# Performance work log

Hardware: AMD Instinct MI355X
Metric: run time of the kernel (lower is better)

The kernel has to match this reference:

```python
import jax, jax.numpy as jnp
import numpy as np

N, E = 50000, 800000
DIN, DH, DOUT = 128, 128, 64


def setup_inputs() -> dict:
    key = jax.random.key(0)
    k = jax.random.split(key, 6)
    node_features = jax.random.normal(k[0], (N, DIN), dtype=jnp.float32)
    edge_src = jax.random.randint(k[1], (E,), 0, N)
    edge_dst = jax.random.randint(k[2], (E,), 0, N)
    # Glorot-ish init for the two GCNConv weight matrices, zero bias (PyG default bias=True)
    W1 = jax.random.normal(k[3], (DIN, DH), dtype=jnp.float32) * (1.0 / np.sqrt(DIN))
    b1 = jnp.zeros((DH,), dtype=jnp.float32)
    W2 = jax.random.normal(k[4], (DH, DOUT), dtype=jnp.float32) * (1.0 / np.sqrt(DH))
    b2 = jnp.zeros((DOUT,), dtype=jnp.float32)
    return {"node_features": node_features, "edge_src": edge_src, "edge_dst": edge_dst,
            "W1": W1, "b1": b1, "W2": W2, "b2": b2}


def gcn_conv(x, W, b, src, dst, n):
    """PyG GCNConv: add self-loops, symmetric D^-1/2 (A+I) D^-1/2 normalization."""
    xw = x @ W  # [n, d_out]
    loops = jnp.arange(n, dtype=src.dtype)
    s = jnp.concatenate([src, loops])  # edges + self-loops
    d = jnp.concatenate([dst, loops])
    deg = jax.ops.segment_sum(jnp.ones_like(d, dtype=xw.dtype), d, num_segments=n)
    dinv = jnp.where(deg > 0, jax.lax.rsqrt(deg), 0.0)
    norm = dinv[s] * dinv[d]  # [E + n]
    msg = xw[s] * norm[:, None]  # gather + scale (memory-bound)
    out = jax.ops.segment_sum(msg, d, num_segments=n)  # scatter-add
    return out + b


def reference(node_features, edge_src, edge_dst, W1, b1, W2, b2):
    n = node_features.shape[0]
    h = gcn_conv(node_features, W1, b1, edge_src, edge_dst, n)
    h = jax.nn.relu(h)  # dropout omitted (inference / eval mode)
    h = gcn_conv(h, W2, b2, edge_src, edge_dst, n)
    # EdgePredictor: per-edge dot product of endpoint representations
    score = jnp.sum(h[edge_src] * h[edge_dst], axis=-1)  # [E]
    return score
```

## Files before the change

kernel.cpp:

```cpp
#include <hip/hip_runtime.h>
#include <hip/hip_bf16.h>
#include <type_traits>


#define DIN 128
#define DH  128
#define DOUT 64
#define BSH 7
#define BNODES 128
#define CAP 2560
#define QSH 13
#define POISON 0xAAAAAAAAu

typedef __attribute__((ext_vector_type(8))) short short8;
typedef __attribute__((ext_vector_type(4))) float floatx4;

__device__ inline float2 bf2_to_f2(unsigned u) {
    union { unsigned i; float f; } a, b;
    a.i = u << 16;
    b.i = u & 0xffff0000u;
    return make_float2(a.f, b.f);
}
__device__ inline float bf_to_f(unsigned short u) {
    union { unsigned i; float f; } a;
    a.i = ((unsigned)u) << 16;
    return a.f;
}
__device__ inline unsigned short f_to_bf(float f) {
    union { float f; unsigned i; } v; v.f = f;
    unsigned r = v.i + 0x7fffu + ((v.i >> 16) & 1u);
    return (unsigned short)(r >> 16);
}

__global__ __launch_bounds__(256) void place_gemm1_kernel(
    const int* __restrict__ src, const int* __restrict__ dst,
    unsigned* __restrict__ cursor, uint2* __restrict__ tmp, int E, int EB,
    const float* __restrict__ X, const float* __restrict__ W1,
    unsigned short* __restrict__ Y, int nrows) {
    __shared__ __align__(16) char smem[69632];
    int bid = blockIdx.x, t = threadIdx.x;

    if (bid < EB) {
        int* hist = (int*)smem;
        int* cur  = hist + 512;
        hist[t] = 0; hist[t + 256] = 0;
        __syncthreads();
        int base = bid * 4096 + t;
        int d[16];
#pragma unroll
        for (int it = 0; it < 16; ++it) {
            int e = base + it * 256;
            d[it] = (e < E) ? dst[e] : -1;
            if (d[it] >= 0) atomicAdd(&hist[d[it] >> BSH], 1);
        }
        __syncthreads();
#pragma unroll
        for (int k = t; k < 512; k += 256)
            if (hist[k])
                cur[k] = (int)(atomicAdd(&cursor[k], (unsigned)hist[k]) - POISON);
        __syncthreads();
#pragma unroll
        for (int it = 0; it < 16; ++it) {
            int e = base + it * 256;
            if (d[it] >= 0) {
                int bkt = d[it] >> BSH;
                int r = atomicAdd(&cur[bkt], 1);
                if (r >= 0 && r < CAP)
                    tmp[(size_t)bkt * CAP + r] =
                        make_uint2((unsigned)src[e] |
                                   ((unsigned)(d[it] & (BNODES - 1)) << 16),
                                   (unsigned)e);
            }
        }
        return;
    }

    constexpr int KP = 136;
    unsigned short* Xs = (unsigned short*)smem;
    unsigned short* Wt = Xs + 128 * KP;
    int row0 = (bid - EB) * 128;

#pragma unroll
    for (int it = 0; it < 16; ++it) {
        int idx = it * 256 + t;
        int r = idx >> 5;
        int c4 = (idx & 31) * 4;
        int gr = row0 + r; if (gr >= nrows) gr = nrows - 1;
        float4 v = *(const float4*)(X + (size_t)gr * 128 + c4);
        ushort4 p;
        p.x = f_to_bf(v.x); p.y = f_to_bf(v.y);
        p.z = f_to_bf(v.z); p.w = f_to_bf(v.w);
        *(ushort4*)&Xs[r * KP + c4] = p;
    }
#pragma unroll
    for (int it = 0; it < 16; ++it) {
        int idx = it * 256 + t;
        int n = idx >> 5;
        int k4 = (idx & 31) * 4;
        ushort4 p;
        p.x = f_to_bf(W1[(size_t)(k4 + 0) * 128 + n]);
        p.y = f_to_bf(W1[(size_t)(k4 + 1) * 128 + n]);
        p.z = f_to_bf(W1[(size_t)(k4 + 2) * 128 + n]);
        p.w = f_to_bf(W1[(size_t)(k4 + 3) * 128 + n]);
        *(ushort4*)&Wt[n * KP + k4] = p;
    }
    __syncthreads();

    int wv = t >> 6, lane = t & 63;
    int lr = lane & 15;
    int lk = (lane >> 4) * 8;
    int rw = wv * 32;

    floatx4 acc[2][8];
#pragma unroll
    for (int rt = 0; rt < 2; ++rt)
#pragma unroll
        for (int ct = 0; ct < 8; ++ct) acc[rt][ct] = (floatx4){0.f, 0.f, 0.f, 0.f};

#pragma unroll
    for (int kk = 0; kk < 128; kk += 32) {
        short8 a[2], b[8];
#pragma unroll
        for (int rt = 0; rt < 2; ++rt)
            a[rt] = *(const short8*)&Xs[(rw + rt * 16 + lr) * KP + kk + lk];
#pragma unroll
        for (int ct = 0; ct < 8; ++ct)
            b[ct] = *(const short8*)&Wt[(ct * 16 + lr) * KP + kk + lk];
#pragma unroll
        for (int rt = 0; rt < 2; ++rt)
#pragma unroll
            for (int ct = 0; ct < 8; ++ct)
                acc[rt][ct] = __builtin_amdgcn_mfma_f32_16x16x32_bf16(
                    a[rt], b[ct], acc[rt][ct], 0, 0, 0);
    }
#pragma unroll
    for (int rt = 0; rt < 2; ++rt) {
#pragma unroll
        for (int i = 0; i < 4; ++i) {
            int grow = row0 + rw + rt * 16 + (lane >> 4) * 4 + i;
            if (grow >= nrows) continue;
#pragma unroll
            for (int ct = 0; ct < 8; ++ct)
                Y[(size_t)grow * 128 + ct * 16 + lr] = f_to_bf(acc[rt][ct][i]);
        }
    }
}

__global__ __launch_bounds__(256) void bucket_csr_kernel(const uint2* __restrict__ tmp,
                                                         const unsigned* __restrict__ cursor,
                                                         int* __restrict__ row_beg,
                                                         int* __restrict__ row_end,
                                                         float* __restrict__ dinv,
                                                         int* __restrict__ col,
                                                         int* __restrict__ eidx, int N) {
    __shared__ int hist[1024], cur[1024];
    __shared__ int tsum[256];
    __shared__ unsigned ebuf[CAP];
    __shared__ unsigned ibuf[CAP];
    __shared__ unsigned ssrc[CAP];
    __shared__ unsigned sidx[CAP];
    int b = blockIdx.x, t = threadIdx.x;
    int size = (int)(cursor[b] - POISON);
    if (size < 0) size = 0;
    if (size > CAP) size = CAP;
    size_t rbase = (size_t)b * CAP;
#pragma unroll
    for (int k = 0; k < 4; ++k) hist[t * 4 + k] = 0;
    __syncthreads();
    for (int i = t; i < size; i += 256) {
        uint2 e = tmp[rbase + i];
        ebuf[i] = e.x;
        ibuf[i] = e.y;
        int key = (int)(e.x >> 16) * 8 + (int)((e.x & 0xffffu) >> QSH);
        atomicAdd(&hist[key], 1);
    }
    __syncthreads();
    int local[4];
    int s = 0;
#pragma unroll
    for (int k = 0; k < 4; ++k) { local[k] = hist[t * 4 + k]; s += local[k]; }
    tsum[t] = s;
    __syncthreads();
    for (int off = 1; off < 256; off <<= 1) {
        int u = (t >= off) ? tsum[t - off] : 0;
        __syncthreads();
        tsum[t] += u;
        __syncthreads();
    }
    int run = tsum[t] - s;
#pragma unroll
    for (int k = 0; k < 4; ++k) {
        hist[t * 4 + k] = run;
        cur[t * 4 + k] = run;
        run += local[k];
    }
    __syncthreads();
    if (t < BNODES) {
        int node = b * BNODES + t;
        if (node < N) {
            int nbeg = hist[t * 8];
            int nend = (t == BNODES - 1) ? size : hist[t * 8 + 8];
            row_beg[node] = (int)rbase + nbeg;
            row_end[node] = (int)rbase + nend;
            dinv[node] = rsqrtf((float)(nend - nbeg + 1));
        }
    }
    __syncthreads();
    for (int i = t; i < size; i += 256) {
        unsigned e = ebuf[i];
        int key = (int)(e >> 16) * 8 + (int)((e & 0xffffu) >> QSH);
        int r = atomicAdd(&cur[key], 1);
        ssrc[r] = e & 0xffffu;
        sidx[r] = ibuf[i];
    }
    __syncthreads();
    for (int i = t; i < size; i += 256) {
        col[rbase + i]  = (int)ssrc[i];
        eidx[rbase + i] = (int)sidx[i];
    }
}

__global__ __launch_bounds__(256) void agg1_kernel(const unsigned short* __restrict__ y1,
                                                   const int* __restrict__ row_beg,
                                                   const int* __restrict__ row_end,
                                                   const int* __restrict__ col,
                                                   const float* __restrict__ dinv,
                                                   const float* __restrict__ b1,
                                                   unsigned short* __restrict__ h1, int n) {
    int w = (blockIdx.x * 256 + threadIdx.x) >> 6;
    int lane = threadIdx.x & 63;
    if (w >= n) return;
    float dw = dinv[w];
    float acc0, acc1;
    {
        float2 t2 = bf2_to_f2(*(const unsigned*)(y1 + (size_t)w * 128 + lane * 2));
        acc0 = dw * t2.x; acc1 = dw * t2.y;
    }
    int beg = row_beg[w], end = row_end[w];
    int i = beg;
    for (; i + 8 <= end; i += 8) {
        int s[8];
#pragma unroll
        for (int u = 0; u < 8; ++u) s[u] = col[i + u];
        float dv[8];
#pragma unroll
        for (int u = 0; u < 8; ++u) dv[u] = dinv[s[u]];
        unsigned tv[8];
#pragma unroll
        for (int u = 0; u < 8; ++u)
            tv[u] = *(const unsigned*)(y1 + (size_t)s[u] * 128 + lane * 2);
#pragma unroll
        for (int u = 0; u < 8; ++u) {
            float2 f = bf2_to_f2(tv[u]);
            acc0 = fmaf(dv[u], f.x, acc0);
            acc1 = fmaf(dv[u], f.y, acc1);
        }
    }
    for (; i < end; ++i) {
        int s = col[i];
        float dv = dinv[s];
        float2 f = bf2_to_f2(*(const unsigned*)(y1 + (size_t)s * 128 + lane * 2));
        acc0 = fmaf(dv, f.x, acc0);
        acc1 = fmaf(dv, f.y, acc1);
    }
    float r0 = fmaxf(fmaf(dw, acc0, b1[lane * 2]), 0.f);
    float r1 = fmaxf(fmaf(dw, acc1, b1[lane * 2 + 1]), 0.f);
    unsigned pk = (unsigned)f_to_bf(r0) | ((unsigned)f_to_bf(r1) << 16);
    *(unsigned*)(h1 + (size_t)w * 128 + lane * 2) = pk;
}

__global__ __launch_bounds__(256) void mfma_gemm2_kernel(const unsigned short* __restrict__ X,
                                                         const float* __restrict__ W,
                                                         const float* __restrict__ dinv,
                                                         unsigned short* __restrict__ Y,
                                                         int nrows) {
    constexpr int KP = 136;
    __shared__ unsigned short Xs[128 * KP];
    __shared__ unsigned short Wt[64 * KP];
    int tid = threadIdx.x;
    int row0 = blockIdx.x * 128;

#pragma unroll
    for (int it = 0; it < 8; ++it) {
        int idx = it * 256 + tid;
        int r = idx >> 4;
        int c8 = (idx & 15) * 8;
        int gr = row0 + r; if (gr >= nrows) gr = nrows - 1;
        uint4 v = *(const uint4*)(X + (size_t)gr * 128 + c8);
        *(uint4*)&Xs[r * KP + c8] = v;
    }
#pragma unroll
    for (int it = 0; it < 8; ++it) {
        int idx = it * 256 + tid;
        int n = idx >> 5;
        int k4 = (idx & 31) * 4;
        ushort4 p;
        p.x = f_to_bf(W[(size_t)(k4 + 0) * 64 + n]);
        p.y = f_to_bf(W[(size_t)(k4 + 1) * 64 + n]);
        p.z = f_to_bf(W[(size_t)(k4 + 2) * 64 + n]);
        p.w = f_to_bf(W[(size_t)(k4 + 3) * 64 + n]);
        *(ushort4*)&Wt[n * KP + k4] = p;
    }
    __syncthreads();

    int wv = tid >> 6, lane = tid & 63;
    int lr = lane & 15;
    int lk = (lane >> 4) * 8;
    int rw = wv * 32;

    floatx4 acc[2][4];
#pragma unroll
    for (int rt = 0; rt < 2; ++rt)
#pragma unroll
        for (int ct = 0; ct < 4; ++ct) acc[rt][ct] = (floatx4){0.f, 0.f, 0.f, 0.f};

#pragma unroll
    for (int kk = 0; kk < 128; kk += 32) {
        short8 a[2], b[4];
#pragma unroll
        for (int rt = 0; rt < 2; ++rt)
            a[rt] = *(const short8*)&Xs[(rw + rt * 16 + lr) * KP + kk + lk];
#pragma unroll
        for (int ct = 0; ct < 4; ++ct)
            b[ct] = *(const short8*)&Wt[(ct * 16 + lr) * KP + kk + lk];
#pragma unroll
        for (int rt = 0; rt < 2; ++rt)
#pragma unroll
            for (int ct = 0; ct < 4; ++ct)
                acc[rt][ct] = __builtin_amdgcn_mfma_f32_16x16x32_bf16(
                    a[rt], b[ct], acc[rt][ct], 0, 0, 0);
    }
#pragma unroll
    for (int rt = 0; rt < 2; ++rt) {
#pragma unroll
        for (int i = 0; i < 4; ++i) {
            int grow = row0 + rw + rt * 16 + (lane >> 4) * 4 + i;
            if (grow >= nrows) continue;
            float dv = dinv[grow];
#pragma unroll
            for (int ct = 0; ct < 4; ++ct)
                Y[(size_t)grow * 64 + ct * 16 + lr] = f_to_bf(acc[rt][ct][i] * dv);
        }
    }
}

__global__ __launch_bounds__(256) void agg2_kernel(const unsigned short* __restrict__ y,
                                                   const int* __restrict__ row_beg,
                                                   const int* __restrict__ row_end,
                                                   const int* __restrict__ col,
                                                   const float* __restrict__ dinv,
                                                   const float* __restrict__ bias,
                                                   unsigned short* __restrict__ out, int n) {
    int w = (blockIdx.x * 256 + threadIdx.x) >> 6;
    int lane = threadIdx.x & 63;
    if (w >= n) return;
    float acc = bf_to_f(y[(size_t)w * 64 + lane]);
    int beg = row_beg[w], end = row_end[w];
    int i = beg;
    for (; i + 8 <= end; i += 8) {
        int s[8];
#pragma unroll
        for (int u = 0; u < 8; ++u) s[u] = col[i + u];
        unsigned short tv[8];
#pragma unroll
        for (int u = 0; u < 8; ++u) tv[u] = y[(size_t)s[u] * 64 + lane];
#pragma unroll
        for (int u = 0; u < 8; ++u) acc += bf_to_f(tv[u]);
    }
    for (; i < end; ++i) acc += bf_to_f(y[(size_t)col[i] * 64 + lane]);
    float r = fmaf(dinv[w], acc, bias[lane]);
    out[(size_t)w * 64 + lane] = f_to_bf(r);
}

__global__ __launch_bounds__(256) void score_csr_kernel(const unsigned short* __restrict__ h2,
                                                        const int* __restrict__ row_beg,
                                                        const int* __restrict__ row_end,
                                                        const int* __restrict__ col,
                                                        const int* __restrict__ eidx,
                                                        float* __restrict__ out, int n) {
    int w = (blockIdx.x * 256 + threadIdx.x) >> 6;
    int lane = threadIdx.x & 63;
    if (w >= n) return;
    int q = lane & 7;
    uint4 hd = *(const uint4*)(h2 + (size_t)w * 64 + q * 8);
    float d0[8];
    { float2 f;
      f = bf2_to_f2(hd.x); d0[0] = f.x; d0[1] = f.y;
      f = bf2_to_f2(hd.y); d0[2] = f.x; d0[3] = f.y;
      f = bf2_to_f2(hd.z); d0[4] = f.x; d0[5] = f.y;
      f = bf2_to_f2(hd.w); d0[6] = f.x; d0[7] = f.y; }
    int beg = row_beg[w], end = row_end[w];
    int g = lane >> 3;
    for (int i = beg; i < end; i += 8) {
        int ei = i + g;
        bool ok = ei < end;
        int s = ok ? col[ei] : 0;
        uint4 hs = *(const uint4*)(h2 + (size_t)s * 64 + q * 8);
        float v = 0.f;
        float2 f;
        f = bf2_to_f2(hs.x); v = fmaf(d0[0], f.x, v); v = fmaf(d0[1], f.y, v);
        f = bf2_to_f2(hs.y); v = fmaf(d0[2], f.x, v); v = fmaf(d0[3], f.y, v);
        f = bf2_to_f2(hs.z); v = fmaf(d0[4], f.x, v); v = fmaf(d0[5], f.y, v);
        f = bf2_to_f2(hs.w); v = fmaf(d0[6], f.x, v); v = fmaf(d0[7], f.y, v);
        v += __shfl_xor(v, 4);
        v += __shfl_xor(v, 2);
        v += __shfl_xor(v, 1);
        if (ok && q == 0) out[eidx[ei]] = v;
    }
}

extern "C" void kernel_launch(void* const* d_in, const int* in_sizes, int n_in,
                              void* d_out, int out_size, void* d_ws, size_t ws_size,
                              hipStream_t stream) {
    const float* X   = (const float*)d_in[0];
    const int*   src = (const int*)d_in[1];
    const int*   dst = (const int*)d_in[2];
    const float* W1  = (const float*)d_in[3];
    const float* b1  = (const float*)d_in[4];
    const float* W2  = (const float*)d_in[5];
    const float* b2  = (const float*)d_in[6];
    float* score = (float*)d_out;

    const int N = in_sizes[0] / DIN;
    const int E = in_sizes[1];
    const int nbuck = (N + BNODES - 1) / BNODES;
    const int EB = (E + 4095) / 4096;
    const int GB = (N + 127) / 128;

    auto align = [](size_t x) { return (x + 255) & ~(size_t)255; };
    char* p = (char*)d_ws;
    unsigned* cursor = (unsigned*)p;        p += align(512 * 4);
    int*   row_beg = (int*)p;               p += align((size_t)N * 4);
    int*   row_end = (int*)p;               p += align((size_t)N * 4);
    float* dinv    = (float*)p;             p += align((size_t)N * 4);
    int*   col     = (int*)p;               p += align((size_t)nbuck * CAP * 4);
    int*   eidx    = (int*)p;               p += align((size_t)nbuck * CAP * 4);
    uint2* tmp     = (uint2*)p;             p += align((size_t)nbuck * CAP * 8);
    unsigned short* y1 = (unsigned short*)p; p += align((size_t)N * DH * 2);
    unsigned short* h1 = (unsigned short*)p; p += align((size_t)N * DH * 2);
    unsigned short* y2 = y1;
    unsigned short* h2 = y1 + (size_t)N * DOUT;

    place_gemm1_kernel<<<EB + GB, 256, 0, stream>>>(src, dst, cursor, tmp, E, EB,
                                                    X, W1, y1, N);
    bucket_csr_kernel<<<nbuck, 256, 0, stream>>>(tmp, cursor, row_beg, row_end,
                                                 dinv, col, eidx, N);

    int agg_blocks = (N + 3) / 4;
    agg1_kernel<<<agg_blocks, 256, 0, stream>>>(y1, row_beg, row_end, col,
                                                dinv, b1, h1, N);

    mfma_gemm2_kernel<<<GB, 256, 0, stream>>>(h1, W2, dinv, y2, N);

    agg2_kernel<<<agg_blocks, 256, 0, stream>>>(y2, row_beg, row_end, col,
                                                dinv, b2, h2, N);
    score_csr_kernel<<<agg_blocks, 256, 0, stream>>>(h2, row_beg, row_end,
                                                     col, eidx, score, N);
}
```

Baseline: 233.2 us.

## Fuse CSR bucket build with first-layer aggregation using global degree atomics

The per-bucket CSR construction kernel and the layer-1 aggregation kernel become one 512-thread kernel. Each block aggregates its own 128 destination nodes straight from the sorted source list still in LDS, instead of reading col back from global memory. Source-node normalisation needs degrees from other buckets, so the placement kernel now also keeps a global per-node in-degree counter with atomics, and source dinv is recomputed on the fly. This removes one launch and one round trip of CSR data through global memory. The cost is extra global atomics in the placement kernel and far fewer blocks for the aggregation work, each wave walking 16 nodes in sequence.

```diff
diff --git a/kernel.cpp b/kernel.cpp
--- a/kernel.cpp
+++ b/kernel.cpp
@@ -34,7 +34,8 @@
 
 __global__ __launch_bounds__(256) void place_gemm1_kernel(
     const int* __restrict__ src, const int* __restrict__ dst,
-    unsigned* __restrict__ cursor, uint2* __restrict__ tmp, int E, int EB,
+    unsigned* __restrict__ cursor, unsigned* __restrict__ deg,
+    uint2* __restrict__ tmp, int E, int EB,
     const float* __restrict__ X, const float* __restrict__ W1,
     unsigned short* __restrict__ Y, int nrows) {
     __shared__ __align__(16) char smem[69632];
@@ -51,7 +52,10 @@
         for (int it = 0; it < 16; ++it) {
             int e = base + it * 256;
             d[it] = (e < E) ? dst[e] : -1;
-            if (d[it] >= 0) atomicAdd(&hist[d[it] >> BSH], 1);
+            if (d[it] >= 0) {
+                atomicAdd(&hist[d[it] >> BSH], 1);
+                atomicAdd(&deg[d[it]], 1u);
+            }
         }
         __syncthreads();
 #pragma unroll
@@ -146,15 +150,15 @@
     }
 }
 
-__global__ __launch_bounds__(256) void bucket_csr_kernel(const uint2* __restrict__ tmp,
-                                                         const unsigned* __restrict__ cursor,
-                                                         int* __restrict__ row_beg,
-                                                         int* __restrict__ row_end,
-                                                         float* __restrict__ dinv,
-                                                         int* __restrict__ col,
-                                                         int* __restrict__ eidx, int N) {
+__global__ __launch_bounds__(512) void csr_agg1_kernel(
+    const uint2* __restrict__ tmp, const unsigned* __restrict__ cursor,
+    const unsigned* __restrict__ deg,
+    int* __restrict__ row_beg, int* __restrict__ row_end,
+    float* __restrict__ dinv, int* __restrict__ col, int* __restrict__ eidx,
+    const unsigned short* __restrict__ y1, const float* __restrict__ b1,
+    unsigned short* __restrict__ h1, int N) {
     __shared__ int hist[1024], cur[1024];
-    __shared__ int tsum[256];
+    __shared__ int tsum[512];
     __shared__ unsigned ebuf[CAP];
     __shared__ unsigned ibuf[CAP];
     __shared__ unsigned ssrc[CAP];
@@ -164,10 +168,9 @@
     if (size < 0) size = 0;
     if (size > CAP) size = CAP;
     size_t rbase = (size_t)b * CAP;
-#pragma unroll
-    for (int k = 0; k < 4; ++k) hist[t * 4 + k] = 0;
-    __syncthreads();
-    for (int i = t; i < size; i += 256) {
+    hist[t] = 0; hist[t + 512] = 0;
+    __syncthreads();
+    for (int i = t; i < size; i += 512) {
         uint2 e = tmp[rbase + i];
         ebuf[i] = e.x;
         ibuf[i] = e.y;
@@ -175,25 +178,19 @@
         atomicAdd(&hist[key], 1);
     }
     __syncthreads();
-    int local[4];
-    int s = 0;
-#pragma unroll
-    for (int k = 0; k < 4; ++k) { local[k] = hist[t * 4 + k]; s += local[k]; }
+    int l0 = hist[t * 2], l1 = hist[t * 2 + 1];
+    int s = l0 + l1;
     tsum[t] = s;
     __syncthreads();
-    for (int off = 1; off < 256; off <<= 1) {
+    for (int off = 1; off < 512; off <<= 1) {
         int u = (t >= off) ? tsum[t - off] : 0;
         __syncthreads();
         tsum[t] += u;
         __syncthreads();
     }
     int run = tsum[t] - s;
-#pragma unroll
-    for (int k = 0; k < 4; ++k) {
-        hist[t * 4 + k] = run;
-        cur[t * 4 + k] = run;
-        run += local[k];
-    }
+    hist[t * 2] = run;       cur[t * 2] = run;
+    hist[t * 2 + 1] = run + l0; cur[t * 2 + 1] = run + l0;
     __syncthreads();
     if (t < BNODES) {
         int node = b * BNODES + t;
@@ -206,7 +203,7 @@
         }
     }
     __syncthreads();
-    for (int i = t; i < size; i += 256) {
+    for (int i = t; i < size; i += 512) {
         unsigned e = ebuf[i];
         int key = (int)(e >> 16) * 8 + (int)((e & 0xffffu) >> QSH);
         int r = atomicAdd(&cur[key], 1);
@@ -214,59 +211,55 @@
         sidx[r] = ibuf[i];
     }
     __syncthreads();
-    for (int i = t; i < size; i += 256) {
+    for (int i = t; i < size; i += 512) {
         col[rbase + i]  = (int)ssrc[i];
         eidx[rbase + i] = (int)sidx[i];
     }
-}
-
-__global__ __launch_bounds__(256) void agg1_kernel(const unsigned short* __restrict__ y1,
-                                                   const int* __restrict__ row_beg,
-                                                   const int* __restrict__ row_end,
-                                                   const int* __restrict__ col,
-                                                   const float* __restrict__ dinv,
-                                                   const float* __restrict__ b1,
-                                                   unsigned short* __restrict__ h1, int n) {
-    int w = (blockIdx.x * 256 + threadIdx.x) >> 6;
-    int lane = threadIdx.x & 63;
-    if (w >= n) return;
-    float dw = dinv[w];
-    float acc0, acc1;
-    {
-        float2 t2 = bf2_to_f2(*(const unsigned*)(y1 + (size_t)w * 128 + lane * 2));
-        acc0 = dw * t2.x; acc1 = dw * t2.y;
-    }
-    int beg = row_beg[w], end = row_end[w];
-    int i = beg;
-    for (; i + 8 <= end; i += 8) {
-        int s[8];
-#pragma unroll
-        for (int u = 0; u < 8; ++u) s[u] = col[i + u];
-        float dv[8];
-#pragma unroll
-        for (int u = 0; u < 8; ++u) dv[u] = dinv[s[u]];
-        unsigned tv[8];
-#pragma unroll
-        for (int u = 0; u < 8; ++u)
-            tv[u] = *(const unsigned*)(y1 + (size_t)s[u] * 128 + lane * 2);
-#pragma unroll
-        for (int u = 0; u < 8; ++u) {
-            float2 f = bf2_to_f2(tv[u]);
-            acc0 = fmaf(dv[u], f.x, acc0);
-            acc1 = fmaf(dv[u], f.y, acc1);
-        }
-    }
-    for (; i < end; ++i) {
-        int s = col[i];
-        float dv = dinv[s];
-        float2 f = bf2_to_f2(*(const unsigned*)(y1 + (size_t)s * 128 + lane * 2));
-        acc0 = fmaf(dv, f.x, acc0);
-        acc1 = fmaf(dv, f.y, acc1);
-    }
-    float r0 = fmaxf(fmaf(dw, acc0, b1[lane * 2]), 0.f);
-    float r1 = fmaxf(fmaf(dw, acc1, b1[lane * 2 + 1]), 0.f);
-    unsigned pk = (unsigned)f_to_bf(r0) | ((unsigned)f_to_bf(r1) << 16);
-    *(unsigned*)(h1 + (size_t)w * 128 + lane * 2) = pk;
+    int wv = t >> 6, lane = t & 63;
+    float bb0 = b1[lane * 2], bb1 = b1[lane * 2 + 1];
+    for (int l = wv; l < BNODES; l += 8) {
+        int node = b * BNODES + l;
+        if (node >= N) break;
+        int nbeg = hist[l * 8];
+        int nend = (l == BNODES - 1) ? size : hist[l * 8 + 8];
+        float dw = rsqrtf((float)(nend - nbeg + 1));
+        float acc0, acc1;
+        {
+            float2 t2 = bf2_to_f2(*(const unsigned*)(y1 + (size_t)node * 128 + lane * 2));
+            acc0 = dw * t2.x; acc1 = dw * t2.y;
+        }
+        int i = nbeg;
+        for (; i + 8 <= nend; i += 8) {
+            int s8[8];
+#pragma unroll
+            for (int u = 0; u < 8; ++u) s8[u] = (int)ssrc[i + u];
+            float dv[8];
+#pragma unroll
+            for (int u = 0; u < 8; ++u)
+                dv[u] = rsqrtf((float)((int)(deg[s8[u]] - POISON) + 1));
+            unsigned tv[8];
+#pragma unroll
+            for (int u = 0; u < 8; ++u)
+                tv[u] = *(const unsigned*)(y1 + (size_t)s8[u] * 128 + lane * 2);
+#pragma unroll
+            for (int u = 0; u < 8; ++u) {
+                float2 f = bf2_to_f2(tv[u]);
+                acc0 = fmaf(dv[u], f.x, acc0);
+                acc1 = fmaf(dv[u], f.y, acc1);
+            }
+        }
+        for (; i < nend; ++i) {
+            int sv = (int)ssrc[i];
+            float dv = rsqrtf((float)((int)(deg[sv] - POISON) + 1));
+            float2 f = bf2_to_f2(*(const unsigned*)(y1 + (size_t)sv * 128 + lane * 2));
+            acc0 = fmaf(dv, f.x, acc0);
+            acc1 = fmaf(dv, f.y, acc1);
+        }
+        float r0 = fmaxf(fmaf(dw, acc0, bb0), 0.f);
+        float r1 = fmaxf(fmaf(dw, acc1, bb1), 0.f);
+        unsigned pk = (unsigned)f_to_bf(r0) | ((unsigned)f_to_bf(r1) << 16);
+        *(unsigned*)(h1 + (size_t)node * 128 + lane * 2) = pk;
+    }
 }
 
 __global__ __launch_bounds__(256) void mfma_gemm2_kernel(const unsigned short* __restrict__ X,
@@ -430,6 +423,7 @@
     auto align = [](size_t x) { return (x + 255) & ~(size_t)255; };
     char* p = (char*)d_ws;
     unsigned* cursor = (unsigned*)p;        p += align(512 * 4);
+    unsigned* deg    = (unsigned*)p;        p += align((size_t)N * 4);
     int*   row_beg = (int*)p;               p += align((size_t)N * 4);
     int*   row_end = (int*)p;               p += align((size_t)N * 4);
     float* dinv    = (float*)p;             p += align((size_t)N * 4);
@@ -441,17 +435,14 @@
     unsigned short* y2 = y1;
     unsigned short* h2 = y1 + (size_t)N * DOUT;
 
-    place_gemm1_kernel<<<EB + GB, 256, 0, stream>>>(src, dst, cursor, tmp, E, EB,
-                                                    X, W1, y1, N);
-    bucket_csr_kernel<<<nbuck, 256, 0, stream>>>(tmp, cursor, row_beg, row_end,
-                                                 dinv, col, eidx, N);
+    place_gemm1_kernel<<<EB + GB, 256, 0, stream>>>(src, dst, cursor, deg, tmp,
+                                                    E, EB, X, W1, y1, N);
+    csr_agg1_kernel<<<nbuck, 512, 0, stream>>>(tmp, cursor, deg, row_beg, row_end,
+                                               dinv, col, eidx, y1, b1, h1, N);
+
+    mfma_gemm2_kernel<<<GB, 256, 0, stream>>>(h1, W2, dinv, y2, N);
 
     int agg_blocks = (N + 3) / 4;
-    agg1_kernel<<<agg_blocks, 256, 0, stream>>>(y1, row_beg, row_end, col,
-                                                dinv, b1, h1, N);
-
-    mfma_gemm2_kernel<<<GB, 256, 0, stream>>>(h1, W2, dinv, y2, N);
-
     agg2_kernel<<<agg_blocks, 256, 0, stream>>>(y2, row_beg, row_end, col,
                                                 dinv, b2, h2, N);
     score_csr_kernel<<<agg_blocks, 256, 0, stream>>>(h2, row_beg, row_end,
```

Measured after the change: 265.8 us. 1.14x slower.
